# Optimization experiments

Hardware: AMD Instinct MI355X
Metric: run time of the kernel (lower is better)

## Reference

```python
import jax, jax.numpy as jnp
import numpy as np

N_NODES = 100000
N_EDGES = 1600000
D_FEAT = 128
HIDDEN = 128
N_CLASSES = 10
N_GRAPHS = 512


def setup_inputs() -> dict:
    key = jax.random.key(0)
    ks = jax.random.split(key, 8)
    x = jax.random.normal(ks[0], (N_NODES, D_FEAT), dtype=jnp.float32)
    edge_index = jax.random.randint(ks[1], (2, N_EDGES), 0, N_NODES, dtype=jnp.int64)
    batch = jnp.sort(jax.random.randint(ks[2], (N_NODES,), 0, N_GRAPHS, dtype=jnp.int64))
    s = 1.0 / np.sqrt(D_FEAT)
    W1 = jax.random.normal(ks[3], (D_FEAT, HIDDEN), dtype=jnp.float32) * s
    W2 = jax.random.normal(ks[4], (HIDDEN, HIDDEN), dtype=jnp.float32) * s
    W3 = jax.random.normal(ks[5], (HIDDEN, HIDDEN), dtype=jnp.float32) * s
    Wl = jax.random.normal(ks[6], (HIDDEN, N_CLASSES), dtype=jnp.float32) * s
    return {
        'x': x, 'edge_index': edge_index, 'batch': batch,
        'W1': W1, 'b1': jnp.zeros((HIDDEN,), jnp.float32),
        'W2': W2, 'b2': jnp.zeros((HIDDEN,), jnp.float32),
        'W3': W3, 'b3': jnp.zeros((HIDDEN,), jnp.float32),
        'Wl': Wl, 'bl': jnp.zeros((N_CLASSES,), jnp.float32),
    }


def _gcn_norm(edge_index, n_nodes):
    # add self-loops + symmetric normalization (PyG GCNConv defaults)
    loop = jnp.arange(n_nodes, dtype=edge_index.dtype)
    src = jnp.concatenate([edge_index[0], loop])
    dst = jnp.concatenate([edge_index[1], loop])
    deg = jax.ops.segment_sum(jnp.ones_like(dst, jnp.float32), dst, num_segments=n_nodes)
    dinv = jnp.where(deg > 0, jax.lax.rsqrt(deg), 0.0)
    norm = dinv[src] * dinv[dst]  # [E+N]
    return src, dst, norm


def _gcn_conv(x, src, dst, norm, W, b, n_nodes):
    h = x @ W                                   # [N, H]
    msg = norm[:, None] * h[src]                # gather + scale, [E+N, H]
    out = jax.ops.segment_sum(msg, dst, num_segments=n_nodes)  # scatter-add
    return out + b


def reference(x, edge_index, batch, W1, b1, W2, b2, W3, b3, Wl, bl):
    n = x.shape[0]
    src, dst, norm = _gcn_norm(edge_index, n)
    h = jax.nn.relu(_gcn_conv(x, src, dst, norm, W1, b1, n))
    h = jax.nn.relu(_gcn_conv(h, src, dst, norm, W2, b2, n))
    h = _gcn_conv(h, src, dst, norm, W3, b3, n)
    # global mean pool over graphs
    sums = jax.ops.segment_sum(h, batch, num_segments=N_GRAPHS)        # [G, H]
    cnts = jax.ops.segment_sum(jnp.ones((n,), jnp.float32), batch, num_segments=N_GRAPHS)
    pooled = sums / jnp.maximum(cnts, 1.0)[:, None]
    # dropout is identity in eval mode
    return pooled @ Wl + bl                                            # [G, C]
```

## Files before the change

kernel.cpp:

```cpp
#include <hip/hip_runtime.h>
#include <cstdint>
#include <cstddef>

typedef _Float16 half8 __attribute__((ext_vector_type(8)));
typedef float    f32x4 __attribute__((ext_vector_type(4)));

#define NBLK 512
#define BSHIFT 8

static __device__ __forceinline__ float4 ld4(const float* p) {
    return *reinterpret_cast<const float4*>(p);
}

static __device__ __forceinline__ void ld8h(const _Float16* p, float* f) {
    half8 v = *reinterpret_cast<const half8*>(p);
#pragma unroll
    for (int k = 0; k < 8; ++k) f[k] = (float)v[k];
}


__global__ __launch_bounds__(256)
void binA_count(const int* __restrict__ dst, int* __restrict__ cntM,
                int e, int nb, int tile) {
    __shared__ int lc[512];
    const int t = threadIdx.x, j = blockIdx.x;
    lc[t] = 0; lc[t + 256] = 0;
    __syncthreads();
    const int lo = j * tile;
    const int hi = min(e, lo + tile);
    const int4* d4 = (const int4*)(dst + lo);
    const int n4 = (hi - lo) >> 2;
    for (int i = t; i < n4; i += 256) {
        int4 q = d4[i];
        atomicAdd(&lc[q.x >> BSHIFT], 1);
        atomicAdd(&lc[q.y >> BSHIFT], 1);
        atomicAdd(&lc[q.z >> BSHIFT], 1);
        atomicAdd(&lc[q.w >> BSHIFT], 1);
    }
    __syncthreads();
    for (int b = t; b < nb; b += 256) cntM[b * NBLK + j] = lc[b];
}

__global__ __launch_bounds__(256)
void scan1_kernel(const int* __restrict__ cnt, int* __restrict__ blockSums, int n) {
    __shared__ int ts[256];
    const int t = threadIdx.x;
    const int base = blockIdx.x * 1024 + t * 4;
    int s = 0;
    if (base + 3 < n) {
        int4 q = *reinterpret_cast<const int4*>(cnt + base);
        s = q.x + q.y + q.z + q.w;
    } else {
#pragma unroll
        for (int j = 0; j < 4; ++j) if (base + j < n) s += cnt[base + j];
    }
    ts[t] = s;
    __syncthreads();
    for (int off = 128; off > 0; off >>= 1) {
        if (t < off) ts[t] += ts[t + off];
        __syncthreads();
    }
    if (t == 0) blockSums[blockIdx.x] = ts[0];
}

__global__ __launch_bounds__(1024)
void scan_top_kernel(const int* __restrict__ blockSums, int* __restrict__ blockOff,
                     int* __restrict__ total, int nb) {
    __shared__ int ls[1024];
    const int t = threadIdx.x;
    ls[t] = (t < nb) ? blockSums[t] : 0;
    __syncthreads();
    for (int off = 1; off < 1024; off <<= 1) {
        int v = (t >= off) ? ls[t - off] : 0;
        __syncthreads();
        ls[t] += v;
        __syncthreads();
    }
    if (t < nb) blockOff[t] = (t == 0) ? 0 : ls[t - 1];
    if (t == 1023) total[0] = ls[1023];
}

__global__ __launch_bounds__(256)
void scan2_kernel(const int* __restrict__ cnt, const int* __restrict__ blockOff,
                  int* __restrict__ outp, int n) {
    __shared__ int ts[256];
    const int t = threadIdx.x;
    const int base = blockIdx.x * 1024 + t * 4;
    int v[4] = {0, 0, 0, 0};
    if (base + 3 < n) {
        int4 q = *reinterpret_cast<const int4*>(cnt + base);
        v[0] = q.x; v[1] = q.y; v[2] = q.z; v[3] = q.w;
    } else {
#pragma unroll
        for (int j = 0; j < 4; ++j) if (base + j < n) v[j] = cnt[base + j];
    }
    int s = v[0] + v[1] + v[2] + v[3];
    ts[t] = s;
    __syncthreads();
    for (int off = 1; off < 256; off <<= 1) {
        int x = (t >= off) ? ts[t - off] : 0;
        __syncthreads();
        ts[t] += x;
        __syncthreads();
    }
    int excl = blockOff[blockIdx.x] + ((t == 0) ? 0 : ts[t - 1]);
#pragma unroll
    for (int j = 0; j < 4; ++j) {
        if (base + j < n) outp[base + j] = excl;
        excl += v[j];
    }
}

__global__ __launch_bounds__(256)
void binA_place(const int* __restrict__ src, const int* __restrict__ dst,
                const int* __restrict__ offM, unsigned* __restrict__ staging,
                int e, int nb, int tile) {
    __shared__ int cur[512];
    const int t = threadIdx.x, j = blockIdx.x;
    for (int b = t; b < nb; b += 256) cur[b] = offM[b * NBLK + j];
    __syncthreads();
    const int lo = j * tile;
    const int hi = min(e, lo + tile);
    const int4* s4 = (const int4*)(src + lo);
    const int4* d4 = (const int4*)(dst + lo);
    const int n4 = (hi - lo) >> 2;
    for (int i = t; i < n4; i += 256) {
        int4 qs = s4[i];
        int4 qd = d4[i];
        int p0 = atomicAdd(&cur[qd.x >> BSHIFT], 1);
        staging[p0] = ((unsigned)qs.x << 8) | (unsigned)(qd.x & 255);
        int p1 = atomicAdd(&cur[qd.y >> BSHIFT], 1);
        staging[p1] = ((unsigned)qs.y << 8) | (unsigned)(qd.y & 255);
        int p2 = atomicAdd(&cur[qd.z >> BSHIFT], 1);
        staging[p2] = ((unsigned)qs.z << 8) | (unsigned)(qd.z & 255);
        int p3 = atomicAdd(&cur[qd.w >> BSHIFT], 1);
        staging[p3] = ((unsigned)qs.w << 8) | (unsigned)(qd.w & 255);
    }
}

__global__ __launch_bounds__(256)
void bucket_rows(const unsigned* __restrict__ staging, const int* __restrict__ offM,
                 int* __restrict__ rowptr, float* __restrict__ dinv,
                 int n, int nb, int e) {
    __shared__ int lc[256];
    __shared__ int ls[256];
    const int b = blockIdx.x, t = threadIdx.x;
    const int base = offM[b * NBLK];
    const int end  = (b + 1 < nb) ? offM[(b + 1) * NBLK] : e;
    const int d0 = b << BSHIFT;
    const int R  = min(n - d0, 256);
    lc[t] = 0;
    __syncthreads();
    for (int i = base + t; i < end; i += 256) atomicAdd(&lc[staging[i] & 255u], 1);
    __syncthreads();
    const int deg = lc[t];
    ls[t] = deg;
    __syncthreads();
    for (int off = 1; off < 256; off <<= 1) {
        int v = (t >= off) ? ls[t - off] : 0;
        __syncthreads();
        ls[t] += v;
        __syncthreads();
    }
    int excl = (t == 0) ? 0 : ls[t - 1];
    if (t < R) {
        rowptr[d0 + t] = base + excl;
        dinv[d0 + t]   = rsqrtf((float)(deg + 1));
    }
    if (b == nb - 1 && t == 0) rowptr[n] = e;
}

__global__ __launch_bounds__(256)
void bucket_scatter(const unsigned* __restrict__ staging, const int* __restrict__ offM,
                    const int* __restrict__ rowptr, const float* __restrict__ dinv,
                    int2* __restrict__ rec, int n, int nb, int e) {
    __shared__ int   cur[256];
    __shared__ float ldv[256];
    const int b = blockIdx.x, t = threadIdx.x;
    const int base = offM[b * NBLK];
    const int end  = (b + 1 < nb) ? offM[(b + 1) * NBLK] : e;
    const int d0 = b << BSHIFT;
    const int R  = min(n - d0, 256);
    if (t < R) {
        cur[t] = rowptr[d0 + t];
        ldv[t] = dinv[d0 + t];
    }
    __syncthreads();
    for (int i = base + t; i < end; i += 256) {
        unsigned q = staging[i];
        int dl = (int)(q & 255u);
        int s  = (int)(q >> 8);
        int pos = atomicAdd(&cur[dl], 1);
        float w = dinv[s] * ldv[dl];
        rec[pos] = make_int2(s, __float_as_int(w));
    }
}

template<int IN32>
__global__ __launch_bounds__(256)
void gemm_mfma_kernel(const void* __restrict__ Xv, const float* __restrict__ W,
                      _Float16* __restrict__ H16, int n) {
    __shared__ _Float16 Wt[128][136];
    __shared__ _Float16 Sw[4][16][136];

    const int t = threadIdx.x;
#pragma unroll
    for (int j = 0; j < 16; ++j) {
        int i4 = t + 256 * j;
        int k  = i4 >> 5;
        int c4 = (i4 & 31) * 4;
        float4 v = ld4(W + (size_t)i4 * 4);
        Wt[c4 + 0][k] = (_Float16)v.x;
        Wt[c4 + 1][k] = (_Float16)v.y;
        Wt[c4 + 2][k] = (_Float16)v.z;
        Wt[c4 + 3][k] = (_Float16)v.w;
    }
    __syncthreads();

    const int wave = t >> 6;
    const int l    = t & 63;
    const int lr   = l & 15;
    const int lk   = l >> 4;
    const int rowA = blockIdx.x * 64 + wave * 16 + lr;

    half8 a[4];
#pragma unroll
    for (int ks = 0; ks < 4; ++ks) {
#pragma unroll
        for (int j = 0; j < 8; ++j) a[ks][j] = (_Float16)0.f;
    }
    if (rowA < n) {
        if (IN32) {
            const float* X = (const float*)Xv;
#pragma unroll
            for (int ks = 0; ks < 4; ++ks) {
                const float* p = X + (size_t)rowA * 128 + ks * 32 + lk * 8;
                float4 f0 = ld4(p);
                float4 f1 = ld4(p + 4);
                a[ks][0] = (_Float16)f0.x; a[ks][1] = (_Float16)f0.y;
                a[ks][2] = (_Float16)f0.z; a[ks][3] = (_Float16)f0.w;
                a[ks][4] = (_Float16)f1.x; a[ks][5] = (_Float16)f1.y;
                a[ks][6] = (_Float16)f1.z; a[ks][7] = (_Float16)f1.w;
            }
        } else {
            const _Float16* X = (const _Float16*)Xv;
#pragma unroll
            for (int ks = 0; ks < 4; ++ks)
                a[ks] = *reinterpret_cast<const half8*>(X + (size_t)rowA * 128 + ks * 32 + lk * 8);
        }
    }

#pragma unroll
    for (int tt = 0; tt < 8; ++tt) {
        f32x4 acc = {0.f, 0.f, 0.f, 0.f};
#pragma unroll
        for (int ks = 0; ks < 4; ++ks) {
            half8 b = *reinterpret_cast<const half8*>(&Wt[tt * 16 + lr][ks * 32 + lk * 8]);
            acc = __builtin_amdgcn_mfma_f32_16x16x32_f16(a[ks], b, acc, 0, 0, 0);
        }
#pragma unroll
        for (int r = 0; r < 4; ++r)
            Sw[wave][lk * 4 + r][tt * 16 + lr] = (_Float16)acc[r];
    }
    __syncthreads();

#pragma unroll
    for (int j = 0; j < 4; ++j) {
        int chunk = l + 64 * j;
        int r  = chunk >> 4;
        int c8 = chunk & 15;
        int gr = blockIdx.x * 64 + wave * 16 + r;
        if (gr < n) {
            half8 v = *reinterpret_cast<const half8*>(&Sw[wave][r][c8 * 8]);
            *reinterpret_cast<half8*>(H16 + (size_t)gr * 128 + c8 * 8) = v;
        }
    }
}

__global__ __launch_bounds__(256)
void gather_kernel(const int* __restrict__ rowptr, const int2* __restrict__ rec,
                   const float* __restrict__ dinv,
                   const _Float16* __restrict__ h16, const float* __restrict__ bias,
                   _Float16* __restrict__ outb, int n, int do_relu) {
    int gid  = blockIdx.x * blockDim.x + threadIdx.x;
    int node = gid >> 4;
    int lane = gid & 15;
    if (node >= n) return;

    int rs = rowptr[node];
    int re = rowptr[node + 1];
    float di = dinv[node];
    const int fo = lane * 8;

    float acc[8];
    {
        float f[8];
        ld8h(h16 + (size_t)node * 128 + fo, f);
        float c = di * di;
#pragma unroll
        for (int k = 0; k < 8; ++k) acc[k] = c * f[k];
    }

    for (int e0 = rs; e0 < re; e0 += 16) {
        int m = re - e0;
        if (m > 16) m = 16;
        int   sI = 0;
        float wI = 0.f;
        if (lane < m) {
            int2 q = rec[e0 + lane];
            sI = q.x;
            wI = __int_as_float(q.y);
        }
        int j = 0;
        for (; j + 3 < m; j += 4) {
            int   s0 = __shfl(sI, j,     16);
            float w0 = __shfl(wI, j,     16);
            int   s1 = __shfl(sI, j + 1, 16);
            float w1 = __shfl(wI, j + 1, 16);
            int   s2 = __shfl(sI, j + 2, 16);
            float w2 = __shfl(wI, j + 2, 16);
            int   s3 = __shfl(sI, j + 3, 16);
            float w3 = __shfl(wI, j + 3, 16);
            float f0[8], f1[8], f2[8], f3[8];
            ld8h(h16 + (size_t)s0 * 128 + fo, f0);
            ld8h(h16 + (size_t)s1 * 128 + fo, f1);
            ld8h(h16 + (size_t)s2 * 128 + fo, f2);
            ld8h(h16 + (size_t)s3 * 128 + fo, f3);
#pragma unroll
            for (int k = 0; k < 8; ++k) {
                acc[k] = fmaf(w0, f0[k], acc[k]);
                acc[k] = fmaf(w1, f1[k], acc[k]);
                acc[k] = fmaf(w2, f2[k], acc[k]);
                acc[k] = fmaf(w3, f3[k], acc[k]);
            }
        }
        for (; j < m; ++j) {
            int   s0 = __shfl(sI, j, 16);
            float w0 = __shfl(wI, j, 16);
            float f0[8];
            ld8h(h16 + (size_t)s0 * 128 + fo, f0);
#pragma unroll
            for (int k = 0; k < 8; ++k) acc[k] = fmaf(w0, f0[k], acc[k]);
        }
    }

    float4 b0 = ld4(bias + fo);
    float4 b1 = ld4(bias + fo + 4);
    acc[0] += b0.x; acc[1] += b0.y; acc[2] += b0.z; acc[3] += b0.w;
    acc[4] += b1.x; acc[5] += b1.y; acc[6] += b1.z; acc[7] += b1.w;
    if (do_relu) {
#pragma unroll
        for (int k = 0; k < 8; ++k) acc[k] = fmaxf(acc[k], 0.f);
    }
    half8 v;
#pragma unroll
    for (int k = 0; k < 8; ++k) v[k] = (_Float16)acc[k];
    *reinterpret_cast<half8*>(outb + (size_t)node * 128 + fo) = v;
}

__global__ __launch_bounds__(256)
void pool_kernel(const _Float16* __restrict__ h, const int* __restrict__ batch,
                 float* __restrict__ pooled, int n) {
    __shared__ f32x4 red[16][34];
    int g = blockIdx.x;
    int lo = 0, hi = n;
    while (lo < hi) { int mid = (lo + hi) >> 1; if (batch[mid] < g) lo = mid + 1; else hi = mid; }
    int start = lo;
    hi = n;
    while (lo < hi) { int mid = (lo + hi) >> 1; if (batch[mid] < g + 1) lo = mid + 1; else hi = mid; }
    int end = lo;

    const int t   = threadIdx.x;
    const int grp = t >> 4;
    const int ln  = t & 15;

    float acc[8] = {0.f, 0.f, 0.f, 0.f, 0.f, 0.f, 0.f, 0.f};
    for (int i = start + grp; i < end; i += 16) {
        float f[8];
        ld8h(h + (size_t)i * 128 + ln * 8, f);
#pragma unroll
        for (int k = 0; k < 8; ++k) acc[k] += f[k];
    }
    red[grp][ln * 2]     = (f32x4){acc[0], acc[1], acc[2], acc[3]};
    red[grp][ln * 2 + 1] = (f32x4){acc[4], acc[5], acc[6], acc[7]};
    __syncthreads();
#pragma unroll
    for (int off = 8; off > 0; off >>= 1) {
        if (grp < off) {
            red[grp][ln * 2]     += red[grp + off][ln * 2];
            red[grp][ln * 2 + 1] += red[grp + off][ln * 2 + 1];
        }
        __syncthreads();
    }
    if (t < 128) {
        float cnt = (float)(end - start);
        pooled[g * 128 + t] = red[0][t >> 2][t & 3] / fmaxf(cnt, 1.0f);
    }
}

__global__ void final_kernel(const float* __restrict__ pooled, const float* __restrict__ Wl,
                             const float* __restrict__ bl, float* __restrict__ out, int n_classes) {
    __shared__ float ps[128];
    int g = blockIdx.x;
    int t = threadIdx.x;
    ps[t]      = pooled[g * 128 + t];
    ps[t + 64] = pooled[g * 128 + 64 + t];
    __syncthreads();
    if (t < n_classes) {
        float acc = bl[t];
        for (int k = 0; k < 128; ++k)
            acc = fmaf(ps[k], Wl[k * n_classes + t], acc);
        out[g * n_classes + t] = acc;
    }
}

extern "C" void kernel_launch(void* const* d_in, const int* in_sizes, int n_in,
                              void* d_out, int out_size, void* d_ws, size_t ws_size,
                              hipStream_t stream) {
    const float* x     = (const float*)d_in[0];
    const int*   ei    = (const int*)d_in[1];
    const int*   batch = (const int*)d_in[2];
    const float* W1 = (const float*)d_in[3];
    const float* b1 = (const float*)d_in[4];
    const float* W2 = (const float*)d_in[5];
    const float* b2 = (const float*)d_in[6];
    const float* W3 = (const float*)d_in[7];
    const float* b3 = (const float*)d_in[8];
    const float* Wl = (const float*)d_in[9];
    const float* bl = (const float*)d_in[10];
    float* out = (float*)d_out;

    const int N = in_sizes[0] / 128;
    const int E = in_sizes[1] / 2;
    const int C = 10;
    const int G = out_size / C;

    const int* srcI = ei;
    const int* dstI = ei + E;

    const int NB   = (N + 255) >> BSHIFT;
    const int M    = NB * NBLK;
    const int TILE = (((E + NBLK - 1) / NBLK) + 3) & ~3;
    const int scanB = (M + 1023) / 1024;

    char* w = (char*)d_ws;
    size_t off = 0;
    auto alloc = [&](size_t bytes) -> void* {
        void* p = w + off;
        off = (off + bytes + 255) & ~(size_t)255;
        return p;
    };

    int*      rowptr    = (int*)alloc((size_t)(N + 1) * 4);
    float*    dinv      = (float*)alloc((size_t)N * 4);
    int2*     rec       = (int2*)alloc((size_t)E * 8);
    unsigned* staging   = (unsigned*)alloc((size_t)E * 4);
    int*      cntM      = (int*)alloc((size_t)M * 4);
    int*      offM      = (int*)alloc((size_t)M * 4);
    int*      blockSums = (int*)alloc((size_t)scanB * 4);
    int*      blockOff  = (int*)alloc((size_t)scanB * 4);
    int*      scrTotal  = (int*)alloc(256);
    _Float16* h16       = (_Float16*)alloc((size_t)N * 128 * 2);
    _Float16* act16     = (_Float16*)alloc((size_t)N * 128 * 2);
    float*    pooled    = (float*)alloc((size_t)G * 128 * 4);

    binA_count<<<NBLK, 256, 0, stream>>>(dstI, cntM, E, NB, TILE);
    scan1_kernel<<<scanB, 256, 0, stream>>>(cntM, blockSums, M);
    scan_top_kernel<<<1, 1024, 0, stream>>>(blockSums, blockOff, scrTotal, scanB);
    scan2_kernel<<<scanB, 256, 0, stream>>>(cntM, blockOff, offM, M);
    binA_place<<<NBLK, 256, 0, stream>>>(srcI, dstI, offM, staging, E, NB, TILE);
    bucket_rows<<<NB, 256, 0, stream>>>(staging, offM, rowptr, dinv, N, NB, E);
    bucket_scatter<<<NB, 256, 0, stream>>>(staging, offM, rowptr, dinv, rec, N, NB, E);

    const int gemmBlocks = (N + 63) / 64;
    const int gathBlocks = (N * 16 + 255) / 256;

    gemm_mfma_kernel<1><<<gemmBlocks, 256, 0, stream>>>(x, W1, h16, N);
    gather_kernel<<<gathBlocks, 256, 0, stream>>>(rowptr, rec, dinv, h16, b1, act16, N, 1);
    gemm_mfma_kernel<0><<<gemmBlocks, 256, 0, stream>>>(act16, W2, h16, N);
    gather_kernel<<<gathBlocks, 256, 0, stream>>>(rowptr, rec, dinv, h16, b2, act16, N, 1);
    gemm_mfma_kernel<0><<<gemmBlocks, 256, 0, stream>>>(act16, W3, h16, N);
    gather_kernel<<<gathBlocks, 256, 0, stream>>>(rowptr, rec, dinv, h16, b3, act16, N, 0);

    pool_kernel<<<G, 256, 0, stream>>>(act16, batch, pooled, N);
    final_kernel<<<G, 64, 0, stream>>>(pooled, Wl, bl, out, C);
}
```

Measured before the change: 353.6 us.

## Fuse CSR row and scatter kernels, store source-only edges, merge pool with classifier

Merges bucket_rows and bucket_scatter into one kernel that keeps the running write cursors in shared memory and writes only the source index per edge, halving the edge record size. The gather kernel now computes the edge weight on the fly from dinv[src]*dinv[node] instead of loading a precomputed weight. The mean-pool and final linear kernels are fused so pooled features never go to global memory. This removes two launches and cuts edge record traffic, at the cost of an extra random dinv load per edge in each of the three gathers.

Result: no change. 347.8 us (median of 2 runs) (-1.6%).

```diff
diff --git a/kernel.cpp b/kernel.cpp
--- a/kernel.cpp
+++ b/kernel.cpp
@@ -139,11 +139,12 @@
 }
 
 __global__ __launch_bounds__(256)
-void bucket_rows(const unsigned* __restrict__ staging, const int* __restrict__ offM,
-                 int* __restrict__ rowptr, float* __restrict__ dinv,
-                 int n, int nb, int e) {
+void bucket_build(const unsigned* __restrict__ staging, const int* __restrict__ offM,
+                  int* __restrict__ rowptr, float* __restrict__ dinv,
+                  int* __restrict__ rec, int n, int nb, int e) {
     __shared__ int lc[256];
     __shared__ int ls[256];
+    __shared__ int cur[256];
     const int b = blockIdx.x, t = threadIdx.x;
     const int base = offM[b * NBLK];
     const int end  = (b + 1 < nb) ? offM[(b + 1) * NBLK] : e;
@@ -167,32 +168,13 @@
         rowptr[d0 + t] = base + excl;
         dinv[d0 + t]   = rsqrtf((float)(deg + 1));
     }
+    cur[t] = base + excl;
     if (b == nb - 1 && t == 0) rowptr[n] = e;
-}
-
-__global__ __launch_bounds__(256)
-void bucket_scatter(const unsigned* __restrict__ staging, const int* __restrict__ offM,
-                    const int* __restrict__ rowptr, const float* __restrict__ dinv,
-                    int2* __restrict__ rec, int n, int nb, int e) {
-    __shared__ int   cur[256];
-    __shared__ float ldv[256];
-    const int b = blockIdx.x, t = threadIdx.x;
-    const int base = offM[b * NBLK];
-    const int end  = (b + 1 < nb) ? offM[(b + 1) * NBLK] : e;
-    const int d0 = b << BSHIFT;
-    const int R  = min(n - d0, 256);
-    if (t < R) {
-        cur[t] = rowptr[d0 + t];
-        ldv[t] = dinv[d0 + t];
-    }
     __syncthreads();
     for (int i = base + t; i < end; i += 256) {
         unsigned q = staging[i];
-        int dl = (int)(q & 255u);
-        int s  = (int)(q >> 8);
-        int pos = atomicAdd(&cur[dl], 1);
-        float w = dinv[s] * ldv[dl];
-        rec[pos] = make_int2(s, __float_as_int(w));
+        int pos = atomicAdd(&cur[q & 255u], 1);
+        rec[pos] = (int)(q >> 8);
     }
 }
 
@@ -278,7 +260,7 @@
 }
 
 __global__ __launch_bounds__(256)
-void gather_kernel(const int* __restrict__ rowptr, const int2* __restrict__ rec,
+void gather_kernel(const int* __restrict__ rowptr, const int* __restrict__ rec,
                    const float* __restrict__ dinv,
                    const _Float16* __restrict__ h16, const float* __restrict__ bias,
                    _Float16* __restrict__ outb, int n, int do_relu) {
@@ -307,9 +289,8 @@
         int   sI = 0;
         float wI = 0.f;
         if (lane < m) {
-            int2 q = rec[e0 + lane];
-            sI = q.x;
-            wI = __int_as_float(q.y);
+            sI = rec[e0 + lane];
+            wI = dinv[sI] * di;
         }
         int j = 0;
         for (; j + 3 < m; j += 4) {
@@ -359,9 +340,11 @@
 }
 
 __global__ __launch_bounds__(256)
-void pool_kernel(const _Float16* __restrict__ h, const int* __restrict__ batch,
-                 float* __restrict__ pooled, int n) {
+void pool_final_kernel(const _Float16* __restrict__ h, const int* __restrict__ batch,
+                       const float* __restrict__ Wl, const float* __restrict__ bl,
+                       float* __restrict__ out, int n, int n_classes) {
     __shared__ f32x4 red[16][34];
+    __shared__ float cpart[10][16];
     int g = blockIdx.x;
     int lo = 0, hi = n;
     while (lo < hi) { int mid = (lo + hi) >> 1; if (batch[mid] < g) lo = mid + 1; else hi = mid; }
@@ -392,25 +375,23 @@
         }
         __syncthreads();
     }
-    if (t < 128) {
-        float cnt = (float)(end - start);
-        pooled[g * 128 + t] = red[0][t >> 2][t & 3] / fmaxf(cnt, 1.0f);
-    }
-}
-
-__global__ void final_kernel(const float* __restrict__ pooled, const float* __restrict__ Wl,
-                             const float* __restrict__ bl, float* __restrict__ out, int n_classes) {
-    __shared__ float ps[128];
-    int g = blockIdx.x;
-    int t = threadIdx.x;
-    ps[t]      = pooled[g * 128 + t];
-    ps[t + 64] = pooled[g * 128 + 64 + t];
+    if (t < n_classes * 16) {
+        const int c = t >> 4;
+        float p = 0.f;
+#pragma unroll
+        for (int k = 0; k < 8; ++k) {
+            int kk = ln * 8 + k;
+            p = fmaf(red[0][kk >> 2][kk & 3], Wl[kk * n_classes + c], p);
+        }
+        cpart[c][ln] = p;
+    }
     __syncthreads();
     if (t < n_classes) {
-        float acc = bl[t];
-        for (int k = 0; k < 128; ++k)
-            acc = fmaf(ps[k], Wl[k * n_classes + t], acc);
-        out[g * n_classes + t] = acc;
+        float s = 0.f;
+#pragma unroll
+        for (int k = 0; k < 16; ++k) s += cpart[t][k];
+        float cnt = fmaxf((float)(end - start), 1.0f);
+        out[g * n_classes + t] = s / cnt + bl[t];
     }
 }
 
@@ -453,7 +434,7 @@
 
     int*      rowptr    = (int*)alloc((size_t)(N + 1) * 4);
     float*    dinv      = (float*)alloc((size_t)N * 4);
-    int2*     rec       = (int2*)alloc((size_t)E * 8);
+    int*      rec       = (int*)alloc((size_t)E * 4);
     unsigned* staging   = (unsigned*)alloc((size_t)E * 4);
     int*      cntM      = (int*)alloc((size_t)M * 4);
     int*      offM      = (int*)alloc((size_t)M * 4);
@@ -462,15 +443,13 @@
     int*      scrTotal  = (int*)alloc(256);
     _Float16* h16       = (_Float16*)alloc((size_t)N * 128 * 2);
     _Float16* act16     = (_Float16*)alloc((size_t)N * 128 * 2);
-    float*    pooled    = (float*)alloc((size_t)G * 128 * 4);
 
     binA_count<<<NBLK, 256, 0, stream>>>(dstI, cntM, E, NB, TILE);
     scan1_kernel<<<scanB, 256, 0, stream>>>(cntM, blockSums, M);
     scan_top_kernel<<<1, 1024, 0, stream>>>(blockSums, blockOff, scrTotal, scanB);
     scan2_kernel<<<scanB, 256, 0, stream>>>(cntM, blockOff, offM, M);
     binA_place<<<NBLK, 256, 0, stream>>>(srcI, dstI, offM, staging, E, NB, TILE);
-    bucket_rows<<<NB, 256, 0, stream>>>(staging, offM, rowptr, dinv, N, NB, E);
-    bucket_scatter<<<NB, 256, 0, stream>>>(staging, offM, rowptr, dinv, rec, N, NB, E);
+    bucket_build<<<NB, 256, 0, stream>>>(staging, offM, rowptr, dinv, rec, N, NB, E);
 
     const int gemmBlocks = (N + 63) / 64;
     const int gathBlocks = (N * 16 + 255) / 256;
@@ -482,6 +461,5 @@
     gemm_mfma_kernel<0><<<gemmBlocks, 256, 0, stream>>>(act16, W3, h16, N);
     gather_kernel<<<gathBlocks, 256, 0, stream>>>(rowptr, rec, dinv, h16, b3, act16, N, 0);
 
-    pool_kernel<<<G, 256, 0, stream>>>(act16, batch, pooled, N);
-    final_kernel<<<G, 64, 0, stream>>>(pooled, Wl, bl, out, C);
-}
+    pool_final_kernel<<<G, 256, 0, stream>>>(act16, batch, Wl, bl, out, N, C);
+}
```
